# Performance work log

Hardware: AMD Instinct MI355X
Metric: run time of the kernel (lower is better)

## Reference

```python
import jax, jax.numpy as jnp
import numpy as np

B, C, H, W, D = 4, 64, 64, 192, 24


def setup_inputs() -> dict:
    key = jax.random.key(0)
    ks = jax.random.split(key, 8)
    x = jax.random.normal(ks[0], (B, C, H, W), dtype=jnp.float32)
    y = jax.random.normal(ks[1], (B, C, H, W), dtype=jnp.float32)
    # disparity coordinate samples: pixel x-coordinates in [0, W-1]
    d1 = jax.random.uniform(ks[2], (B, D, H, W), dtype=jnp.float32) * (W - 1.0)
    d2 = jax.random.uniform(ks[3], (B, D, H, W), dtype=jnp.float32) * (W - 1.0)
    s = 1.0 / np.sqrt(C)
    qw = jax.random.normal(ks[4], (C, C), dtype=jnp.float32) * s
    qb = jax.random.normal(ks[5], (C,), dtype=jnp.float32) * 0.01
    kw = jax.random.normal(ks[6], (C, C), dtype=jnp.float32) * s
    kb = jax.random.normal(ks[7], (C,), dtype=jnp.float32) * 0.01
    return {"x": x, "y": y, "disp_range_samples1": d1, "disp_range_samples2": d2,
            "ndisp": D, "qw": qw, "qb": qb, "kw": kw, "kb": kb}


def _conv1x1(x, w, b):
    return jnp.einsum('oi,bihw->bohw', w, x) + b[None, :, None, None]


def _cost_volume(Q, K, disp_x):
    """mean_c( Q * grid_sample(K, bilinear, zeros, align_corners=False) ).
    Q,K: [B,C,H,W]; disp_x: [B,D,H,W] pixel x-coords. Returns [B,D,H,W]."""
    b, c, h, w = K.shape
    # torch grid_sample(align_corners=False) unnormalization of
    # coords = pix/((dim-1)/2)-1  ->  pix*dim/(dim-1) - 0.5
    xs = disp_x * (w / (w - 1.0)) - 0.5                      # [B,D,H,W]
    ys_row = jnp.arange(h, dtype=xs.dtype) * (h / (h - 1.0)) - 0.5
    ys = jnp.broadcast_to(ys_row[None, None, :, None], xs.shape)
    x0 = jnp.floor(xs)
    y0 = jnp.floor(ys)
    tx = xs - x0
    ty = ys - y0
    x0i = x0.astype(jnp.int32)
    y0i = y0.astype(jnp.int32)

    def corner(dy, dx, wgt):
        yi = y0i + dy
        xi = x0i + dx
        valid = ((yi >= 0) & (yi < h) & (xi >= 0) & (xi < w)).astype(Q.dtype)
        yc = jnp.clip(yi, 0, h - 1)
        xc = jnp.clip(xi, 0, w - 1)
        # per-batch gather: [C,H,W] indexed by [D,H,W] -> [C,D,H,W]
        g = jax.vmap(lambda im, yy, xx: im[:, yy, xx])(K, yc, xc)  # [B,C,D,H,W]
        return jnp.einsum('bchw,bcdhw->bdhw', Q, g * (wgt * valid)[:, None])

    cost = (corner(0, 0, (1.0 - ty) * (1.0 - tx)) +
            corner(0, 1, (1.0 - ty) * tx) +
            corner(1, 0, ty * (1.0 - tx)) +
            corner(1, 1, ty * tx))
    return cost / c


def reference(x, y, disp_range_samples1, disp_range_samples2, ndisp, qw, qb, kw, kb):
    assert ndisp == disp_range_samples1.shape[1]
    Q1 = _conv1x1(x, qw, qb)
    K1 = _conv1x1(y, kw, kb)
    cost1 = _cost_volume(Q1, K1, disp_range_samples1)
    Q2 = _conv1x1(y, qw, qb)
    K2 = _conv1x1(x, kw, kb)
    cost2 = _cost_volume(Q2, K2, disp_range_samples2)
    return (cost1, cost2)
```

## Files before the change

### kernel.cpp

```cpp
#include <hip/hip_runtime.h>
#include <stdint.h>

#define BB 4
#define CC 64
#define HH 64
#define WW 192
#define DD 24
#define HWQ (HH * WW)
#define PIX (BB * HWQ)

typedef __attribute__((ext_vector_type(8))) short short8;
typedef __attribute__((ext_vector_type(4))) float floatx4;

__device__ __forceinline__ float bf1(uint16_t u) {
    union { uint32_t i; float f; } c; c.i = ((uint32_t)u) << 16; return c.f;
}
__device__ __forceinline__ uint16_t f2bf(float f) {
    union { float f; uint32_t i; } c; c.f = f;
    uint32_t u = c.i;
    return (uint16_t)((u + 0x7fffu + ((u >> 16) & 1u)) >> 16);
}

#define A_SHORTS ((size_t)2 * PIX * CC)
#define S_F32OFF 4240

__global__ __launch_bounds__(64) void prep_kernel(
    const float* __restrict__ qw, const float* __restrict__ qb,
    const float* __restrict__ kw, const float* __restrict__ kb,
    float* __restrict__ fws) {
    const int bid = blockIdx.x;
    const int j   = threadIdx.x;
    if (bid < 64) {
        float acc = 0.f;
#pragma unroll 8
        for (int c = 0; c < CC; c++)
            acc = fmaf(qw[c * CC + bid], kw[c * CC + j], acc);
        fws[bid * 64 + j] = acc;
    } else if (bid == 64) {
        float bt = 0.f;
#pragma unroll 8
        for (int c = 0; c < CC; c++) bt = fmaf(qb[c], kw[c * CC + j], bt);
        fws[4096 + j] = bt;
        if (j == 0) {
            float g = 0.f;
#pragma unroll 8
            for (int c = 0; c < CC; c++) g = fmaf(qb[c], kb[c], g);
            fws[4224] = g;
        }
    } else {
        float al = 0.f;
#pragma unroll 8
        for (int c = 0; c < CC; c++) al = fmaf(qw[c * CC + j], kb[c], al);
        fws[4160 + j] = al;
    }
}

__global__ __launch_bounds__(256) void convA_kernel(
    const float* __restrict__ x, const float* __restrict__ y,
    float* __restrict__ fws, uint16_t* __restrict__ A,
    uint16_t* __restrict__ Ybf) {
    const int v = blockIdx.y;
    const float* src = v ? y : x;
    float* s = fws + S_F32OFF;

    __shared__ float wt[64][64];
    __shared__ float bs[64], al[64];
    __shared__ float gm;
    const int tid = threadIdx.y * 64 + threadIdx.x;
    for (int idx = tid; idx < 4096; idx += 256) wt[idx >> 6][idx & 63] = fws[idx];
    if (tid < 64) { bs[tid] = fws[4096 + tid]; al[tid] = fws[4160 + tid]; }
    if (tid == 64) gm = fws[4224];
    __syncthreads();

    const int pix0 = blockIdx.x * 128 + threadIdx.x * 2;
    const int b    = pix0 / HWQ;
    const int hw0  = pix0 - b * HWQ;
    const int j0   = threadIdx.y * 16;

    float acc[2][16];
#pragma unroll
    for (int p = 0; p < 2; p++)
#pragma unroll
        for (int k = 0; k < 16; k++) acc[p][k] = bs[j0 + k];
    float sac[2] = {gm, gm};

    const float*    sp   = src + (size_t)b * CC * HWQ + hw0;
    uint16_t*       Ymir = Ybf + (size_t)v * PIX * CC + (size_t)b * CC * HWQ + hw0;
#pragma unroll 4
    for (int i = 0; i < 64; i++) {
        float2 raw = *reinterpret_cast<const float2*>(sp + (size_t)i * HWQ);
        if ((i & 3) == threadIdx.y) {
            uint32_t pv = (uint32_t)f2bf(raw.x) | ((uint32_t)f2bf(raw.y) << 16);
            *reinterpret_cast<uint32_t*>(Ymir + (size_t)i * HWQ) = pv;
        }
        const float* wr = &wt[i][j0];
        const float av = al[i];
        sac[0] = fmaf(raw.x, av, sac[0]);
        sac[1] = fmaf(raw.y, av, sac[1]);
#pragma unroll
        for (int k = 0; k < 16; k++) {
            float wv = wr[k];
            acc[0][k] = fmaf(raw.x, wv, acc[0][k]);
            acc[1][k] = fmaf(raw.y, wv, acc[1][k]);
        }
    }

    uint16_t* dstv = A + (size_t)v * PIX * CC;
#pragma unroll
    for (int p = 0; p < 2; p++) {
        uint32_t pk[8];
#pragma unroll
        for (int k = 0; k < 8; k++)
            pk[k] = (uint32_t)f2bf(acc[p][2 * k]) | ((uint32_t)f2bf(acc[p][2 * k + 1]) << 16);
        uint16_t* dp = dstv + (size_t)(pix0 + p) * CC + j0;
        uint4 lo; lo.x = pk[0]; lo.y = pk[1]; lo.z = pk[2]; lo.w = pk[3];
        uint4 hi; hi.x = pk[4]; hi.y = pk[5]; hi.z = pk[6]; hi.w = pk[7];
        *reinterpret_cast<uint4*>(dp)     = lo;
        *reinterpret_cast<uint4*>(dp + 8) = hi;
    }
    if (threadIdx.y == 0) {
        float2 sv; sv.x = sac[0]; sv.y = sac[1];
        *reinterpret_cast<float2*>(s + (size_t)v * PIX + pix0) = sv;
    }
}

__global__ __launch_bounds__(1024) void cost_kernel(
    const float* __restrict__ disp1, const float* __restrict__ disp2,
    const uint16_t* __restrict__ A, const uint16_t* __restrict__ Ybf,
    const float* __restrict__ fws, float* __restrict__ out) {
    const int h = blockIdx.x;
    const int b = blockIdx.y;
    const int v = blockIdx.z;

    const int       tsel = v ? 0 : 1;
    const float*    disp = v ? disp2 : disp1;
    const uint16_t* Ab   = A + ((size_t)v * PIX + (size_t)b * HWQ + h * WW) * CC;
    const float*    sb   = fws + S_F32OFF + (size_t)v * PIX + (size_t)b * HWQ + h * WW;

    const float ys  = (float)h * (float)(64.0 / 63.0) - 0.5f;
    const float y0f = floorf(ys);
    const float ty  = ys - y0f;
    const int   y0  = (int)y0f;
    const int   y1  = y0 + 1;
    const float vy0 = (y0 >= 0 && y0 < HH) ? 1.f : 0.f;
    const float vy1 = (y1 >= 0 && y1 < HH) ? 1.f : 0.f;
    const int   y0c = min(max(y0, 0), HH - 1);
    const int   y1c = min(max(y1, 0), HH - 1);
    const float ey0 = (1.f - ty) * vy0;
    const float ey1 = ty * vy1;
    const float eysum = ey0 + ey1;

    __shared__ uint16_t Yc[192 * 68];
    __shared__ uint16_t Pt[96 * 196];

    const int tid  = threadIdx.x;
    const int wave = tid >> 6;
    const int lane = tid & 63;
    const int lq   = lane >> 4;
    const int ln   = lane & 15;

    short8 a0f[2], a1f[2];
    if (wave < 12) {
        const int mcl = wave >> 1;
#pragma unroll
        for (int hf = 0; hf < 2; hf++) {
            const uint16_t* ar = Ab + (size_t)(hf * 96 + mcl * 16 + ln) * CC + lq * 8;
            a0f[hf] = *reinterpret_cast<const short8*>(ar);
            a1f[hf] = *reinterpret_cast<const short8*>(ar + 32);
        }
    }

    float dpre[2][3], spre[2][3];
#pragma unroll
    for (int hf = 0; hf < 2; hf++)
#pragma unroll
        for (int q = 0; q < 3; q++) { dpre[hf][q] = 0.f; spre[hf][q] = 0.f; }
#pragma unroll
    for (int hf = 0; hf < 2; hf++) {
#pragma unroll
        for (int q = 0; q < 3; q++) {
            const int o = tid + q * 1024;
            if (o < 96 * DD) {
                const int wl = o % 96;
                const int d  = o / 96;
                const int w  = hf * 96 + wl;
                dpre[hf][q] = disp[((size_t)(b * DD + d) * HH + h) * WW + w];
                spre[hf][q] = sb[w];
            }
        }
    }

    const uint16_t* Yb0 = Ybf + (size_t)tsel * PIX * CC + (size_t)b * CC * HWQ + y0c * WW;
    const uint16_t* Yb1 = Ybf + (size_t)tsel * PIX * CC + (size_t)b * CC * HWQ + y1c * WW;
#pragma unroll
    for (int k = 0; k < 3; k++) {
        const int cg = wave;
        const int xx = k * 64 + lane;
        uint32_t pk[2];
#pragma unroll
        for (int half = 0; half < 2; half++) {
            uint32_t pv = 0;
#pragma unroll
            for (int j = 0; j < 2; j++) {
                const int c = cg * 4 + half * 2 + j;
                const float v0 = bf1(Yb0[(size_t)c * HWQ + xx]);
                const float v1 = bf1(Yb1[(size_t)c * HWQ + xx]);
                const float cb = fmaf(ey1, v1, ey0 * v0);
                pv |= ((uint32_t)f2bf(cb)) << (16 * j);
            }
            pk[half] = pv;
        }
        *reinterpret_cast<uint2*>(&Yc[xx * 68 + cg * 4]) = *reinterpret_cast<uint2*>(pk);
    }
    __syncthreads();

    const float cx = (float)(192.0 / 191.0);
    const float inv_c = 1.f / 64.f;

#pragma unroll
    for (int half = 0; half < 2; half++) {
        if (wave < 12) {
            const int mcl = wave >> 1;
            const short8 a0 = a0f[half];
            const short8 a1 = a1f[half];
#pragma unroll
            for (int i = 0; i < 6; i++) {
                const int nt = (wave & 1) * 6 + i;
                const int Rb = nt * 16;
                const uint16_t* yrow = &Yc[(Rb + ln) * 68 + lq * 8];
                short8 b0, b1;
                *reinterpret_cast<uint2*>(&b0)       = *reinterpret_cast<const uint2*>(yrow);
                *(reinterpret_cast<uint2*>(&b0) + 1) = *reinterpret_cast<const uint2*>(yrow + 4);
                *reinterpret_cast<uint2*>(&b1)       = *reinterpret_cast<const uint2*>(yrow + 32);
                *(reinterpret_cast<uint2*>(&b1) + 1) = *reinterpret_cast<const uint2*>(yrow + 36);
                floatx4 acc = {0.f, 0.f, 0.f, 0.f};
                acc = __builtin_amdgcn_mfma_f32_16x16x32_bf16(a0, b0, acc, 0, 0, 0);
                acc = __builtin_amdgcn_mfma_f32_16x16x32_bf16(a1, b1, acc, 0, 0, 0);
                const int pcol = Rb + ln;
                const int wl   = mcl * 16 + lq * 4;
                Pt[(wl + 0) * 196 + pcol] = f2bf(acc[0]);
                Pt[(wl + 1) * 196 + pcol] = f2bf(acc[1]);
                Pt[(wl + 2) * 196 + pcol] = f2bf(acc[2]);
                Pt[(wl + 3) * 196 + pcol] = f2bf(acc[3]);
            }
        }
        __syncthreads();

#pragma unroll
        for (int q = 0; q < 3; q++) {
            const int o = tid + q * 1024;
            if (o < 96 * DD) {
                const int wl = o % 96;
                const int d  = o / 96;
                const int w  = half * 96 + wl;
                const float dsv = dpre[half][q];
                const float xs  = dsv * cx - 0.5f;
                const float x0f = floorf(xs);
                const float tx  = xs - x0f;
                const int   x0  = (int)x0f;
                const int   x1  = x0 + 1;
                const float vx0 = (x0 >= 0 && x0 < WW) ? 1.f : 0.f;
                const float vx1 = (x1 >= 0 && x1 < WW) ? 1.f : 0.f;
                const int   x0c = min(max(x0, 0), WW - 1);
                const int   x1c = min(max(x1, 0), WW - 1);
                const float wx0 = (1.f - tx) * vx0;
                const float wx1 = tx * vx1;
                const float pc0 = bf1(Pt[wl * 196 + x0c]);
                const float pc1 = bf1(Pt[wl * 196 + x1c]);
                const float res = wx0 * pc0 + wx1 * pc1 + spre[half][q] * (eysum * (wx0 + wx1));
                out[(((size_t)(v * BB + b) * DD + d) * HH + h) * WW + w] = res * inv_c;
            }
        }
        if (half == 0) __syncthreads();
    }
}

extern "C" void kernel_launch(void* const* d_in, const int* in_sizes, int n_in,
                              void* d_out, int out_size, void* d_ws, size_t ws_size,
                              hipStream_t stream) {
    const float* x  = (const float*)d_in[0];
    const float* y  = (const float*)d_in[1];
    const float* d1 = (const float*)d_in[2];
    const float* d2 = (const float*)d_in[3];
    const float* qw = (const float*)d_in[5];
    const float* qb = (const float*)d_in[6];
    const float* kw = (const float*)d_in[7];
    const float* kb = (const float*)d_in[8];

    uint16_t* A   = (uint16_t*)d_ws;
    uint16_t* Ybf = (uint16_t*)d_ws + A_SHORTS;
    float*    fws = (float*)((uint16_t*)d_ws + 2 * A_SHORTS);
    float*    out = (float*)d_out;

    prep_kernel<<<dim3(66), dim3(64), 0, stream>>>(qw, qb, kw, kb, fws);
    convA_kernel<<<dim3(PIX / 128, 2), dim3(64, 4), 0, stream>>>(x, y, fws, A, Ybf);
    cost_kernel<<<dim3(HH, BB, 2), dim3(1024), 0, stream>>>(d1, d2, A, Ybf, fws, out);
}
```

Measured before the change: 128.1 us.

## Fuse projection conv into cost kernel, reading raw fp32 inputs directly

Removes the separate convA kernel and its bf16 workspace intermediates (A and Ybf). The cost kernel now computes the fused Q^T K projection per row in registers from the raw fp32 inputs, using the prep weights staged in LDS. It also reads the two needed K-source rows directly as fp32, and one spare set of waves computes the bias term into LDS. This saves a launch and the global round trip of the intermediates, at the cost of recomputing from fp32 inputs with larger reads and extra per-block ALU work in the cost kernel.

```diff
diff --git a/kernel.cpp b/kernel.cpp
--- a/kernel.cpp
+++ b/kernel.cpp
@@ -21,8 +21,6 @@
     return (uint16_t)((u + 0x7fffu + ((u >> 16) & 1u)) >> 16);
 }
 
-#define A_SHORTS ((size_t)2 * PIX * CC)
-#define S_F32OFF 4240
 
 __global__ __launch_bounds__(64) void prep_kernel(
     const float* __restrict__ qw, const float* __restrict__ qb,
@@ -55,87 +53,17 @@
     }
 }
 
-__global__ __launch_bounds__(256) void convA_kernel(
+__global__ __launch_bounds__(1024) void fused_kernel(
     const float* __restrict__ x, const float* __restrict__ y,
-    float* __restrict__ fws, uint16_t* __restrict__ A,
-    uint16_t* __restrict__ Ybf) {
-    const int v = blockIdx.y;
-    const float* src = v ? y : x;
-    float* s = fws + S_F32OFF;
-
-    __shared__ float wt[64][64];
-    __shared__ float bs[64], al[64];
-    __shared__ float gm;
-    const int tid = threadIdx.y * 64 + threadIdx.x;
-    for (int idx = tid; idx < 4096; idx += 256) wt[idx >> 6][idx & 63] = fws[idx];
-    if (tid < 64) { bs[tid] = fws[4096 + tid]; al[tid] = fws[4160 + tid]; }
-    if (tid == 64) gm = fws[4224];
-    __syncthreads();
-
-    const int pix0 = blockIdx.x * 128 + threadIdx.x * 2;
-    const int b    = pix0 / HWQ;
-    const int hw0  = pix0 - b * HWQ;
-    const int j0   = threadIdx.y * 16;
-
-    float acc[2][16];
-#pragma unroll
-    for (int p = 0; p < 2; p++)
-#pragma unroll
-        for (int k = 0; k < 16; k++) acc[p][k] = bs[j0 + k];
-    float sac[2] = {gm, gm};
-
-    const float*    sp   = src + (size_t)b * CC * HWQ + hw0;
-    uint16_t*       Ymir = Ybf + (size_t)v * PIX * CC + (size_t)b * CC * HWQ + hw0;
-#pragma unroll 4
-    for (int i = 0; i < 64; i++) {
-        float2 raw = *reinterpret_cast<const float2*>(sp + (size_t)i * HWQ);
-        if ((i & 3) == threadIdx.y) {
-            uint32_t pv = (uint32_t)f2bf(raw.x) | ((uint32_t)f2bf(raw.y) << 16);
-            *reinterpret_cast<uint32_t*>(Ymir + (size_t)i * HWQ) = pv;
-        }
-        const float* wr = &wt[i][j0];
-        const float av = al[i];
-        sac[0] = fmaf(raw.x, av, sac[0]);
-        sac[1] = fmaf(raw.y, av, sac[1]);
-#pragma unroll
-        for (int k = 0; k < 16; k++) {
-            float wv = wr[k];
-            acc[0][k] = fmaf(raw.x, wv, acc[0][k]);
-            acc[1][k] = fmaf(raw.y, wv, acc[1][k]);
-        }
-    }
-
-    uint16_t* dstv = A + (size_t)v * PIX * CC;
-#pragma unroll
-    for (int p = 0; p < 2; p++) {
-        uint32_t pk[8];
-#pragma unroll
-        for (int k = 0; k < 8; k++)
-            pk[k] = (uint32_t)f2bf(acc[p][2 * k]) | ((uint32_t)f2bf(acc[p][2 * k + 1]) << 16);
-        uint16_t* dp = dstv + (size_t)(pix0 + p) * CC + j0;
-        uint4 lo; lo.x = pk[0]; lo.y = pk[1]; lo.z = pk[2]; lo.w = pk[3];
-        uint4 hi; hi.x = pk[4]; hi.y = pk[5]; hi.z = pk[6]; hi.w = pk[7];
-        *reinterpret_cast<uint4*>(dp)     = lo;
-        *reinterpret_cast<uint4*>(dp + 8) = hi;
-    }
-    if (threadIdx.y == 0) {
-        float2 sv; sv.x = sac[0]; sv.y = sac[1];
-        *reinterpret_cast<float2*>(s + (size_t)v * PIX + pix0) = sv;
-    }
-}
-
-__global__ __launch_bounds__(1024) void cost_kernel(
     const float* __restrict__ disp1, const float* __restrict__ disp2,
-    const uint16_t* __restrict__ A, const uint16_t* __restrict__ Ybf,
     const float* __restrict__ fws, float* __restrict__ out) {
     const int h = blockIdx.x;
     const int b = blockIdx.y;
     const int v = blockIdx.z;
 
-    const int       tsel = v ? 0 : 1;
-    const float*    disp = v ? disp2 : disp1;
-    const uint16_t* Ab   = A + ((size_t)v * PIX + (size_t)b * HWQ + h * WW) * CC;
-    const float*    sb   = fws + S_F32OFF + (size_t)v * PIX + (size_t)b * HWQ + h * WW;
+    const float* qsrc = (v ? y : x) + (size_t)b * CC * HWQ + h * WW;
+    const float* ksrc = (v ? x : y) + (size_t)b * CC * HWQ;
+    const float* disp = v ? disp2 : disp1;
 
     const float ys  = (float)h * (float)(64.0 / 63.0) - 0.5f;
     const float y0f = floorf(ys);
@@ -150,8 +78,11 @@
     const float ey1 = ty * vy1;
     const float eysum = ey0 + ey1;
 
+    __shared__ uint32_t PtGbuf[96 * 196 / 2];
     __shared__ uint16_t Yc[192 * 68];
-    __shared__ uint16_t Pt[96 * 196];
+    __shared__ float    s_lds[192];
+    uint16_t* Pt = (uint16_t*)PtGbuf;
+    float*    Gf = (float*)PtGbuf;
 
     const int tid  = threadIdx.x;
     const int wave = tid >> 6;
@@ -159,58 +90,100 @@
     const int lq   = lane >> 4;
     const int ln   = lane & 15;
 
+    for (int idx = tid; idx < 4225; idx += 1024) Gf[idx] = fws[idx];
+
+    float dpre[2][3];
+#pragma unroll
+    for (int hf = 0; hf < 2; hf++)
+#pragma unroll
+        for (int q = 0; q < 3; q++) {
+            const int o = tid + q * 1024;
+            dpre[hf][q] = 0.f;
+            if (o < 96 * DD) {
+                const int wl = o % 96;
+                const int d  = o / 96;
+                dpre[hf][q] = disp[((size_t)(b * DD + d) * HH + h) * WW + (hf * 96 + wl)];
+            }
+        }
+
+    const float* yb0 = ksrc + (size_t)y0c * WW;
+    const float* yb1 = ksrc + (size_t)y1c * WW;
+    float yv0[3][2][2], yv1[3][2][2];
+#pragma unroll
+    for (int k = 0; k < 3; k++) {
+        const int xx = k * 64 + lane;
+#pragma unroll
+        for (int hf = 0; hf < 2; hf++)
+#pragma unroll
+            for (int j = 0; j < 2; j++) {
+                const int c = wave * 4 + hf * 2 + j;
+                yv0[k][hf][j] = yb0[(size_t)c * HWQ + xx];
+                yv1[k][hf][j] = yb1[(size_t)c * HWQ + xx];
+            }
+    }
+
+    __syncthreads();
+
     short8 a0f[2], a1f[2];
     if (wave < 12) {
         const int mcl = wave >> 1;
 #pragma unroll
         for (int hf = 0; hf < 2; hf++) {
-            const uint16_t* ar = Ab + (size_t)(hf * 96 + mcl * 16 + ln) * CC + lq * 8;
-            a0f[hf] = *reinterpret_cast<const short8*>(ar);
-            a1f[hf] = *reinterpret_cast<const short8*>(ar + 32);
-        }
-    }
-
-    float dpre[2][3], spre[2][3];
-#pragma unroll
-    for (int hf = 0; hf < 2; hf++)
-#pragma unroll
-        for (int q = 0; q < 3; q++) { dpre[hf][q] = 0.f; spre[hf][q] = 0.f; }
-#pragma unroll
-    for (int hf = 0; hf < 2; hf++) {
-#pragma unroll
-        for (int q = 0; q < 3; q++) {
-            const int o = tid + q * 1024;
-            if (o < 96 * DD) {
-                const int wl = o % 96;
-                const int d  = o / 96;
-                const int w  = hf * 96 + wl;
-                dpre[hf][q] = disp[((size_t)(b * DD + d) * HH + h) * WW + w];
-                spre[hf][q] = sb[w];
-            }
-        }
-    }
-
-    const uint16_t* Yb0 = Ybf + (size_t)tsel * PIX * CC + (size_t)b * CC * HWQ + y0c * WW;
-    const uint16_t* Yb1 = Ybf + (size_t)tsel * PIX * CC + (size_t)b * CC * HWQ + y1c * WW;
+            const int wloc = hf * 96 + mcl * 16 + ln;
+            const float* xp = qsrc + wloc;
+            float acc0[8], acc1[8];
+#pragma unroll
+            for (int k = 0; k < 8; k++) {
+                acc0[k] = Gf[4096 + lq * 8 + k];
+                acc1[k] = Gf[4096 + lq * 8 + 32 + k];
+            }
+#pragma unroll 4
+            for (int i = 0; i < 64; i++) {
+                const float xv = xp[(size_t)i * HWQ];
+                const float* g = &Gf[i * 64 + lq * 8];
+#pragma unroll
+                for (int k = 0; k < 8; k++) {
+                    acc0[k] = fmaf(xv, g[k],      acc0[k]);
+                    acc1[k] = fmaf(xv, g[k + 32], acc1[k]);
+                }
+            }
+            short8 A0, A1;
+#pragma unroll
+            for (int k = 0; k < 8; k++) {
+                A0[k] = (short)f2bf(acc0[k]);
+                A1[k] = (short)f2bf(acc1[k]);
+            }
+            a0f[hf] = A0;
+            a1f[hf] = A1;
+        }
+    } else {
+        const int w = tid - 768;
+        if (w < 192) {
+            float sac = Gf[4224];
+#pragma unroll 4
+            for (int i = 0; i < 64; i++)
+                sac = fmaf(qsrc[(size_t)i * HWQ + w], Gf[4160 + i], sac);
+            s_lds[w] = sac;
+        }
+    }
+
 #pragma unroll
     for (int k = 0; k < 3; k++) {
-        const int cg = wave;
         const int xx = k * 64 + lane;
         uint32_t pk[2];
 #pragma unroll
-        for (int half = 0; half < 2; half++) {
+        for (int hf = 0; hf < 2; hf++) {
             uint32_t pv = 0;
 #pragma unroll
             for (int j = 0; j < 2; j++) {
-                const int c = cg * 4 + half * 2 + j;
-                const float v0 = bf1(Yb0[(size_t)c * HWQ + xx]);
-                const float v1 = bf1(Yb1[(size_t)c * HWQ + xx]);
+                const float v0 = bf1(f2bf(yv0[k][hf][j]));
+                const float v1 = bf1(f2bf(yv1[k][hf][j]));
                 const float cb = fmaf(ey1, v1, ey0 * v0);
                 pv |= ((uint32_t)f2bf(cb)) << (16 * j);
             }
-            pk[half] = pv;
-        }
-        *reinterpret_cast<uint2*>(&Yc[xx * 68 + cg * 4]) = *reinterpret_cast<uint2*>(pk);
+            pk[hf] = pv;
+        }
+        *reinterpret_cast<uint2*>(&Yc[xx * 68 + wave * 4]) = *reinterpret_cast<uint2*>(pk);
     }
     __syncthreads();
 
@@ -267,7 +240,7 @@
                 const float wx1 = tx * vx1;
                 const float pc0 = bf1(Pt[wl * 196 + x0c]);
                 const float pc1 = bf1(Pt[wl * 196 + x1c]);
-                const float res = wx0 * pc0 + wx1 * pc1 + spre[half][q] * (eysum * (wx0 + wx1));
+                const float res = wx0 * pc0 + wx1 * pc1 + s_lds[w] * (eysum * (wx0 + wx1));
                 out[(((size_t)(v * BB + b) * DD + d) * HH + h) * WW + w] = res * inv_c;
             }
         }
@@ -287,12 +260,9 @@
     const float* kw = (const float*)d_in[7];
     const float* kb = (const float*)d_in[8];
 
-    uint16_t* A   = (uint16_t*)d_ws;
-    uint16_t* Ybf = (uint16_t*)d_ws + A_SHORTS;
-    float*    fws = (float*)((uint16_t*)d_ws + 2 * A_SHORTS);
-    float*    out = (float*)d_out;
+    float* fws = (float*)d_ws;
+    float* out = (float*)d_out;
 
     prep_kernel<<<dim3(66), dim3(64), 0, stream>>>(qw, qb, kw, kb, fws);
-    convA_kernel<<<dim3(PIX / 128, 2), dim3(64, 4), 0, stream>>>(x, y, fws, A, Ybf);
-    cost_kernel<<<dim3(HH, BB, 2), dim3(1024), 0, stream>>>(d1, d2, A, Ybf, fws, out);
-}
+    fused_kernel<<<dim3(HH, BB, 2), dim3(1024), 0, stream>>>(x, y, d1, d2, fws, out);
+}
```

After: 149.5 us. 1.17x slower.
